# Kernel tuning notes

Measured on AMD Instinct MI355X. Metric: run time of the kernel, lower is better.

Reference implementation:

```python
import jax, jax.numpy as jnp
import numpy as np

EMBED = 2048
NH = 16          # query heads (x2 for diff pairs)
NKV = 8          # kv heads
DEPTH = 12
HD = EMBED // NH // 2   # 64
NREP = NH // NKV        # 2
SCALING = HD ** -0.5
LAMBDA_INIT = 1.0 - 0.65 * float(np.exp(-0.35 * DEPTH))
EPS = 1e-5


def setup_inputs() -> dict:
    key = jax.random.key(0)
    ks = jax.random.split(key, 12)
    T, B = 2048, 2
    x = jax.random.normal(ks[0], (T, B, EMBED), jnp.float32)
    # interleaved rotary tables over full head_dim (HD), HD/2 frequencies
    inv_freq = 1.0 / (10000.0 ** (np.arange(0, HD, 2, dtype=np.float32) / HD))
    ang = np.arange(T, dtype=np.float32)[:, None] * inv_freq[None, :]  # (T, HD/2)
    cos = jnp.asarray(np.cos(ang), jnp.float32)
    sin = jnp.asarray(np.sin(ang), jnp.float32)
    s = EMBED ** -0.5
    Wq = jax.random.normal(ks[1], (EMBED, EMBED), jnp.float32) * s
    Wk = jax.random.normal(ks[2], (EMBED, EMBED // NREP), jnp.float32) * s
    Wv = jax.random.normal(ks[3], (EMBED, EMBED // NREP), jnp.float32) * s
    Wo = jax.random.normal(ks[4], (EMBED, EMBED), jnp.float32) * s
    lq1 = jax.random.normal(ks[5], (HD,), jnp.float32) * 0.1
    lk1 = jax.random.normal(ks[6], (HD,), jnp.float32) * 0.1
    lq2 = jax.random.normal(ks[7], (HD,), jnp.float32) * 0.1
    lk2 = jax.random.normal(ks[8], (HD,), jnp.float32) * 0.1
    g = jnp.ones((2 * HD,), jnp.float32)  # RMSNorm affine weight
    return {"x": x, "cos": cos, "sin": sin, "Wq": Wq, "Wk": Wk, "Wv": Wv,
            "Wo": Wo, "lq1": lq1, "lk1": lk1, "lq2": lq2, "lk2": lk2, "g": g}


def _rope_interleaved(t, cos, sin):
    # t: (B, T, H, HD); cos/sin: (T, HD/2). Pairs are (even, odd) lanes.
    x1 = t[..., 0::2]
    x2 = t[..., 1::2]
    c = cos[None, :, None, :]
    s = sin[None, :, None, :]
    o1 = x1 * c - x2 * s
    o2 = x1 * s + x2 * c
    return jnp.stack([o1, o2], axis=-1).reshape(t.shape)


def reference(x, cos, sin, Wq, Wk, Wv, Wo, lq1, lk1, lq2, lk2, g):
    T, B, E = x.shape
    # projections (torch code reshapes (T,B,E) contiguously into (B,T,...))
    q = (x @ Wq).reshape(B, T, 2 * NH, HD)
    k = (x @ Wk).reshape(B, T, 2 * NKV, HD)
    v = (x @ Wv).reshape(B, T, NKV, 2 * HD)
    q = _rope_interleaved(q, cos, sin)
    k = _rope_interleaved(k, cos, sin)
    q = jnp.transpose(q, (0, 2, 1, 3)) * SCALING      # (B, 2NH, T, HD)
    k = jnp.repeat(jnp.transpose(k, (0, 2, 1, 3)), NREP, axis=1)  # (B, 2NH, T, HD)
    v = jnp.repeat(jnp.transpose(v, (0, 2, 1, 3)), NREP, axis=1)  # (B, NH, T, 2HD)
    aw = jnp.einsum('bhtd,bhsd->bhts', q, k)          # (B, 2NH, T, T)
    mask = jnp.triu(jnp.full((T, T), -jnp.inf, aw.dtype), 1)
    aw = jax.nn.softmax(jnp.nan_to_num(aw) + mask, axis=-1)
    lam = jnp.exp(jnp.sum(lq1 * lk1)) - jnp.exp(jnp.sum(lq2 * lk2)) + LAMBDA_INIT
    aw = aw.reshape(B, NH, 2, T, T)
    diff = aw[:, :, 0] - lam * aw[:, :, 1]            # (B, NH, T, T)
    attn = jnp.einsum('bhts,bhsd->bhtd', diff, v)     # (B, NH, T, 2HD)
    # sublayer RMSNorm over 2*HD, then scale by (1 - lambda_init)
    rms = jnp.sqrt(jnp.mean(attn * attn, axis=-1, keepdims=True) + EPS)
    attn = (attn / rms) * g * (1.0 - LAMBDA_INIT)
    attn = jnp.transpose(attn, (0, 2, 1, 3)).reshape(B, T, NH * 2 * HD)
    return attn @ Wo  # (B, T, E)
```

## Files before the change

kernel.cpp:

```cpp
#include <hip/hip_runtime.h>
#include <math.h>

typedef __attribute__((ext_vector_type(4))) float f32x4;
typedef __attribute__((ext_vector_type(8))) short short8;
typedef __attribute__((ext_vector_type(4))) short short4v;

#define LAM_INIT 0.9902528750666895f
#define ONE_M_LI 0.0097471249333105f
#define QSCALE   0.18033688011112042f

static __device__ __forceinline__ float bs2f(short s) {
  union { unsigned u; float f; } c;
  c.u = ((unsigned)(unsigned short)s) << 16;
  return c.f;
}
static __device__ __forceinline__ short f2bs(float f) {
  union { float f; unsigned u; } c; c.f = f;
  unsigned r = c.u + 0x7fffu + ((c.u >> 16) & 1u);
  return (short)(r >> 16);
}
static __device__ __forceinline__ short f2bs_fast(float f) {
  union { float f; unsigned u; } c; c.f = f;
  return (short)((c.u + 0x8000u) >> 16);
}
static __device__ __forceinline__ void gld16(const void* g, void* l) {
  __builtin_amdgcn_global_load_lds(
      (const __attribute__((address_space(1))) void*)g,
      (__attribute__((address_space(3))) void*)l, 16, 0, 0);
}
#if __has_builtin(__builtin_amdgcn_exp2f)
#define EXP2F(x) __builtin_amdgcn_exp2f(x)
#else
#define EXP2F(x) exp2f(x)
#endif

__global__ void cast_x(const float* __restrict__ x, short* __restrict__ xb, int n) {
  int i = (blockIdx.x * 256 + threadIdx.x) * 4;
  if (i < n) {
    float4 v = *(const float4*)(x + i);
    short4v o;
    o[0] = f2bs(v.x); o[1] = f2bs(v.y); o[2] = f2bs(v.z); o[3] = f2bs(v.w);
    *(short4v*)(xb + i) = o;
  }
}

__global__ void transpose_cast(const float* __restrict__ src, short* __restrict__ dst,
                               int srcCols, int dstRowOff, int dstLd) {
  __shared__ float tile[32][33];
  int c0 = blockIdx.x * 32, r0 = blockIdx.y * 32;
  int tx = threadIdx.x, ty = threadIdx.y;
#pragma unroll
  for (int i = 0; i < 32; i += 8)
    tile[ty + i][tx] = src[(long)(r0 + ty + i) * srcCols + c0 + tx];
  __syncthreads();
#pragma unroll
  for (int i = 0; i < 32; i += 8)
    dst[(long)(dstRowOff + c0 + ty + i) * dstLd + r0 + tx] = f2bs(tile[tx][ty + i]);
}

template<int BF16OUT>
__global__ __launch_bounds__(256)
void gemm_bt(const short* __restrict__ A, const short* __restrict__ Bt,
             void* __restrict__ Cp, int K, int N) {
  __shared__ __align__(16) short As[128 * 32];
  __shared__ __align__(16) short Bs[128 * 32];
  const int tid  = threadIdx.x;
  const int lane = tid & 63;
  const int wave = tid >> 6;
  const long mBase = (long)blockIdx.y * 128;
  const long nBase = (long)blockIdx.x * 128;
  const int wm = (wave >> 1) * 64;
  const int wn = (wave & 1) * 64;

  f32x4 acc[4][4];
#pragma unroll
  for (int i = 0; i < 4; i++)
#pragma unroll
    for (int j = 0; j < 4; j++)
#pragma unroll
      for (int r = 0; r < 4; r++) acc[i][j][r] = 0.f;

  const int r0  = tid >> 2;
  const int kp0 = (tid & 3) * 8;
  const short* a0 = A  + (mBase + r0) * K + kp0;
  const short* a1 = A  + (mBase + r0 + 64) * K + kp0;
  const short* b0 = Bt + (nBase + r0) * K + kp0;
  const short* b1 = Bt + (nBase + r0 + 64) * K + kp0;
  short* AsW = As + wave * 512;
  short* BsW = Bs + wave * 512;

  const int mr = wm + (lane & 15);
  const int nr = wn + (lane & 15);
  const int kr = (lane >> 4) * 8;

  for (int kt = 0; kt < K; kt += 32) {
    __syncthreads();
    gld16(a0 + kt, AsW);
    gld16(a1 + kt, AsW + 2048);
    gld16(b0 + kt, BsW);
    gld16(b1 + kt, BsW + 2048);
    __syncthreads();
    short8 af[4], bf[4];
#pragma unroll
    for (int mt = 0; mt < 4; mt++) af[mt] = *(const short8*)&As[(mr + mt * 16) * 32 + kr];
#pragma unroll
    for (int nt = 0; nt < 4; nt++) bf[nt] = *(const short8*)&Bs[(nr + nt * 16) * 32 + kr];
#pragma unroll
    for (int mt = 0; mt < 4; mt++)
#pragma unroll
      for (int nt = 0; nt < 4; nt++)
        acc[mt][nt] = __builtin_amdgcn_mfma_f32_16x16x32_bf16(af[mt], bf[nt], acc[mt][nt], 0, 0, 0);
  }

  const long col0 = nBase + wn + (lane & 15);
  const long row0 = mBase + wm + (lane >> 4) * 4;
#pragma unroll
  for (int mt = 0; mt < 4; mt++)
#pragma unroll
    for (int nt = 0; nt < 4; nt++)
#pragma unroll
      for (int rg = 0; rg < 4; rg++) {
        long idx = (row0 + mt * 16 + rg) * N + col0 + nt * 16;
        if (BF16OUT) ((short*)Cp)[idx] = f2bs(acc[mt][nt][rg]);
        else         ((float*)Cp)[idx] = acc[mt][nt][rg];
      }
}

__global__ __launch_bounds__(256) void rope_q(short* __restrict__ QKV,
    const float* __restrict__ cosp, const float* __restrict__ sinp) {
  int idx = blockIdx.x * 256 + threadIdx.x;
  int r = idx >> 8;
  int col = (idx & 255) * 8;
  short* p = QKV + (long)r * 4096 + col;
  short8 v = *(const short8*)p;
  int pos = r & 2047;
  int f0 = (col & 63) >> 1;
  float4 c = *(const float4*)(cosp + pos * 32 + f0);
  float4 s = *(const float4*)(sinp + pos * 32 + f0);
  float cc[4] = {c.x, c.y, c.z, c.w};
  float ss[4] = {s.x, s.y, s.z, s.w};
  short8 o;
#pragma unroll
  for (int j = 0; j < 4; j++) {
    float x0 = bs2f(v[2 * j]), x1 = bs2f(v[2 * j + 1]);
    o[2 * j]     = f2bs((x0 * cc[j] - x1 * ss[j]) * QSCALE);
    o[2 * j + 1] = f2bs((x0 * ss[j] + x1 * cc[j]) * QSCALE);
  }
  *(short8*)p = o;
}

__global__ __launch_bounds__(256) void repack_k(const short* __restrict__ QKV,
    const float* __restrict__ cosp, const float* __restrict__ sinp,
    short* __restrict__ Kt) {
  const int stile = blockIdx.x, h = blockIdx.y, b = blockIdx.z;
  short* dst = Kt + (long)((b * 16 + h) * 32 + stile) * 4096;
#pragma unroll
  for (int half = 0; half < 2; half++) {
    int o8 = threadIdx.x + half * 256;
    int r = o8 & 15, c = (o8 >> 4) & 3, ks = (o8 >> 6) & 1, gq = o8 >> 7;
    int t = stile * 64 + gq * 16 + r;
    const short* src = QKV + ((long)(b * 2048 + t)) * 4096 + 2048 + h * 64 + ks * 32 + c * 8;
    short8 v = *(const short8*)src;
    const float* cp = cosp + t * 32 + ks * 16 + c * 4;
    const float* sp = sinp + t * 32 + ks * 16 + c * 4;
    short8 o;
#pragma unroll
    for (int j = 0; j < 4; j++) {
      float x0 = bs2f(v[2 * j]), x1 = bs2f(v[2 * j + 1]);
      o[2 * j]     = f2bs(x0 * cp[j] - x1 * sp[j]);
      o[2 * j + 1] = f2bs(x0 * sp[j] + x1 * cp[j]);
    }
    *(short8*)(dst + o8 * 8) = o;
  }
}

__global__ __launch_bounds__(256) void repack_v(const short* __restrict__ QKV,
                                                short* __restrict__ Vt) {
  __shared__ short Ts[64][130];
  const int tid = threadIdx.x;
  const int stile = blockIdx.x, kv = blockIdx.y, b = blockIdx.z;
#pragma unroll
  for (int half = 0; half < 2; half++) {
    int trow = half * 32 + (tid >> 3);
    int hwc = (tid & 7) * 16;
    const short* src = QKV + ((long)(b * 2048 + stile * 64 + trow)) * 4096 + 3072 + kv * 128 + hwc;
    *(short8*)&Ts[trow][hwc]     = *(const short8*)src;
    *(short8*)&Ts[trow][hwc + 8] = *(const short8*)(src + 8);
  }
  __syncthreads();
  short* dst = Vt + (long)((b * 8 + kv) * 32 + stile) * 8192;
#pragma unroll
  for (int k4 = 0; k4 < 4; k4++) {
    int o8 = tid + k4 * 256;
    int r = o8 & 15, c = (o8 >> 4) & 3, ks = (o8 >> 6) & 1, gq = o8 >> 7;
    int tt = ks * 32 + c * 8;
    int dv = gq * 16 + r;
    short8 o;
#pragma unroll
    for (int j = 0; j < 8; j++) o[j] = Ts[tt + j][dv];
    *(short8*)(dst + o8 * 8) = o;
  }
}

__global__ __launch_bounds__(256, 2)
void diffattn(const short* __restrict__ QKV, const short* __restrict__ Kt,
              const short* __restrict__ Vt,
              const float* __restrict__ lq1, const float* __restrict__ lk1,
              const float* __restrict__ lq2, const float* __restrict__ lk2,
              const float* __restrict__ g, short* __restrict__ attnp) {
  __shared__ __align__(16) short Ks[2][4096];
  __shared__ __align__(16) short Vs[2][8192];
  __shared__ __align__(16) short Ps[4][2][16][72];

  const int tid  = threadIdx.x;
  const int lane = tid & 63;
  const int wave = tid >> 6;
  const int quad = lane >> 4;
  const int l15  = lane & 15;

  const int bx   = blockIdx.x;
  const int xcd  = bx & 7;
  const int slot = bx >> 3;
  const int hb   = xcd * 4 + (slot & 3);
  const int h    = hb & 15;
  const int b    = hb >> 4;
  const int qb   = 31 - (slot >> 2);
  const long rowBase = (long)b * 2048;

  float lam;
  {
    float v1 = lq1[lane] * lk1[lane];
    float v2 = lq2[lane] * lk2[lane];
#pragma unroll
    for (int m = 32; m >= 1; m >>= 1) { v1 += __shfl_xor(v1, m); v2 += __shfl_xor(v2, m); }
    lam = __expf(v1) - __expf(v2) + LAM_INIT;
  }

  const int tq = qb * 64 + wave * 16 + l15;
  short8 qf[2][2];
#pragma unroll
  for (int hd = 0; hd < 2; hd++)
#pragma unroll
    for (int ks = 0; ks < 2; ks++)
      qf[hd][ks] = *(const short8*)(QKV + (rowBase + tq) * 4096 + (2 * h + hd) * 64 + ks * 32 + quad * 8);

  const short* KtB = Kt + (long)((b * 16 + h) * 32) * 4096;
  const short* VtB = Vt + (long)((b * 8 + (h >> 1)) * 32) * 8192;
  short* KsB = &Ks[0][0];
  short* VsB = &Vs[0][0];

#define STAGE(ST, BUF) do {                                                  \
    const short* kg_ = KtB + (long)(ST) * 4096 + wave * 1024 + lane * 8;     \
    const short* vg_ = VtB + (long)(ST) * 8192 + wave * 2048 + lane * 8;     \
    short* kl_ = KsB + (BUF) * 4096 + wave * 1024;                           \
    short* vl_ = VsB + (BUF) * 8192 + wave * 2048;                           \
    gld16(kg_,        kl_);                                                  \
    gld16(kg_ + 512,  kl_ + 512);                                            \
    gld16(vg_,        vl_);                                                  \
    gld16(vg_ + 512,  vl_ + 512);                                            \
    gld16(vg_ + 1024, vl_ + 1024);                                           \
    gld16(vg_ + 1536, vl_ + 1536);                                           \
  } while (0)

  float lS[2][4];
  f32x4 oA[2][8];
#pragma unroll
  for (int hd = 0; hd < 2; hd++) {
#pragma unroll
    for (int r = 0; r < 4; r++) lS[hd][r] = 0.f;
#pragma unroll
    for (int ot = 0; ot < 8; ot++)
#pragma unroll
      for (int r = 0; r < 4; r++) oA[hd][ot][r] = 0.f;
  }

  STAGE(0, 0);

  for (int st = 0; st <= qb; st++) {
    const int buf = st & 1;
    __syncthreads();
    if (st < qb) STAGE(st + 1, buf ^ 1);

    const short* Ktile = KsB + buf * 4096;
    const short* Vtile = VsB + buf * 8192;

    f32x4 sc[2][4];
#pragma unroll
    for (int hd = 0; hd < 2; hd++)
#pragma unroll
      for (int nt = 0; nt < 4; nt++)
#pragma unroll
        for (int r = 0; r < 4; r++) sc[hd][nt][r] = 0.f;
#pragma unroll
    for (int ks = 0; ks < 2; ks++) {
      short8 kf[4];
#pragma unroll
      for (int nt = 0; nt < 4; nt++)
        kf[nt] = *(const short8*)(Ktile + (nt * 2 + ks) * 512 + lane * 8);
#pragma unroll
      for (int nt = 0; nt < 4; nt++) {
        sc[0][nt] = __builtin_amdgcn_mfma_f32_16x16x32_bf16(qf[0][ks], kf[nt], sc[0][nt], 0, 0, 0);
        sc[1][nt] = __builtin_amdgcn_mfma_f32_16x16x32_bf16(qf[1][ks], kf[nt], sc[1][nt], 0, 0, 0);
      }
    }

    const bool diag = (st == qb);
    const int tg = qb * 64 + wave * 16 + quad * 4;
#pragma unroll
    for (int hd = 0; hd < 2; hd++)
#pragma unroll
      for (int nt = 0; nt < 4; nt++) {
        const int sg = st * 64 + nt * 16 + l15;
#pragma unroll
        for (int r = 0; r < 4; r++) {
          float p = EXP2F(sc[hd][nt][r]);
          if (diag && (sg > tg + r)) p = 0.f;
          lS[hd][r] += p;
          Ps[wave][hd][quad * 4 + r][nt * 16 + l15] = f2bs_fast(p);
        }
      }

#pragma unroll
    for (int ks = 0; ks < 2; ks++) {
      short8 p0 = *(const short8*)&Ps[wave][0][l15][ks * 32 + quad * 8];
      short8 p1 = *(const short8*)&Ps[wave][1][l15][ks * 32 + quad * 8];
#pragma unroll
      for (int ot = 0; ot < 8; ot++) {
        short8 vf = *(const short8*)(Vtile + (ot * 2 + ks) * 512 + lane * 8);
        oA[0][ot] = __builtin_amdgcn_mfma_f32_16x16x32_bf16(p0, vf, oA[0][ot], 0, 0, 0);
        oA[1][ot] = __builtin_amdgcn_mfma_f32_16x16x32_bf16(p1, vf, oA[1][ot], 0, 0, 0);
      }
    }
  }
#undef STAGE

#pragma unroll
  for (int hd = 0; hd < 2; hd++)
#pragma unroll
    for (int r = 0; r < 4; r++) {
      float t = lS[hd][r];
      t += __shfl_xor(t, 1); t += __shfl_xor(t, 2);
      t += __shfl_xor(t, 4); t += __shfl_xor(t, 8);
      lS[hd][r] = t;
    }
  float i1[4], i2[4], ssq[4];
#pragma unroll
  for (int r = 0; r < 4; r++) { i1[r] = 1.f / lS[0][r]; i2[r] = lam / lS[1][r]; ssq[r] = 0.f; }
#pragma unroll
  for (int ot = 0; ot < 8; ot++)
#pragma unroll
    for (int r = 0; r < 4; r++) {
      float d = oA[0][ot][r] * i1[r] - oA[1][ot][r] * i2[r];
      oA[0][ot][r] = d;
      ssq[r] += d * d;
    }
#pragma unroll
  for (int r = 0; r < 4; r++) {
    float t = ssq[r];
    t += __shfl_xor(t, 1); t += __shfl_xor(t, 2);
    t += __shfl_xor(t, 4); t += __shfl_xor(t, 8);
    ssq[r] = ONE_M_LI / sqrtf(t * (1.f / 128.f) + 1e-5f);
  }
  const long orow = rowBase + qb * 64 + wave * 16 + quad * 4;
#pragma unroll
  for (int ot = 0; ot < 8; ot++) {
    const float gv = g[ot * 16 + l15];
#pragma unroll
    for (int r = 0; r < 4; r++)
      attnp[(orow + r) * 2048 + h * 128 + ot * 16 + l15] = f2bs(oA[0][ot][r] * ssq[r] * gv);
  }
}

extern "C" void kernel_launch(void* const* d_in, const int* in_sizes, int n_in,
                              void* d_out, int out_size, void* d_ws, size_t ws_size,
                              hipStream_t stream) {
  const float* x    = (const float*)d_in[0];
  const float* cosp = (const float*)d_in[1];
  const float* sinp = (const float*)d_in[2];
  const float* Wq   = (const float*)d_in[3];
  const float* Wk   = (const float*)d_in[4];
  const float* Wv   = (const float*)d_in[5];
  const float* Wo   = (const float*)d_in[6];
  const float* lq1  = (const float*)d_in[7];
  const float* lk1  = (const float*)d_in[8];
  const float* lq2  = (const float*)d_in[9];
  const float* lk2  = (const float*)d_in[10];
  const float* g    = (const float*)d_in[11];
  float* out = (float*)d_out;

  const size_t MB = 1u << 20;
  char* ws = (char*)d_ws;
  short* xb    = (short*)(ws);
  short* Kt    = (short*)(ws);
  short* Vt    = (short*)(ws + 8 * MB);
  short* Wqkvt = (short*)(ws + 16 * MB);
  short* Wot   = (short*)(ws + 32 * MB);
  short* QKVb  = (short*)(ws + 40 * MB);
  short* attnp = (short*)(ws + 72 * MB);

  cast_x<<<8192, 256, 0, stream>>>(x, xb, 8388608);
  dim3 tb(32, 8);
  transpose_cast<<<dim3(64, 64), tb, 0, stream>>>(Wq, Wqkvt, 2048, 0, 2048);
  transpose_cast<<<dim3(32, 64), tb, 0, stream>>>(Wk, Wqkvt, 1024, 2048, 2048);
  transpose_cast<<<dim3(32, 64), tb, 0, stream>>>(Wv, Wqkvt, 1024, 3072, 2048);
  transpose_cast<<<dim3(64, 64), tb, 0, stream>>>(Wo, Wot, 2048, 0, 2048);

  gemm_bt<1><<<dim3(32, 32), 256, 0, stream>>>(xb, Wqkvt, QKVb, 2048, 4096);
  rope_q<<<4096, 256, 0, stream>>>(QKVb, cosp, sinp);
  repack_k<<<dim3(32, 16, 2), 256, 0, stream>>>(QKVb, cosp, sinp, Kt);
  repack_v<<<dim3(32, 8, 2), 256, 0, stream>>>(QKVb, Vt);
  diffattn<<<1024, 256, 0, stream>>>(QKVb, Kt, Vt, lq1, lk1, lq2, lk2, g, attnp);
  gemm_bt<0><<<dim3(16, 32), 256, 0, stream>>>(attnp, Wot, out, 2048, 2048);
}
```

Before: 382.3 us.

## Merge weight transposes and K/V repacks, add XCD-aware GEMM tile mapping

```diff
diff --git a/kernel.cpp b/kernel.cpp
--- a/kernel.cpp
+++ b/kernel.cpp
@@ -44,9 +44,16 @@
   }
 }
 
-__global__ void transpose_cast(const float* __restrict__ src, short* __restrict__ dst,
-                               int srcCols, int dstRowOff, int dstLd) {
+__global__ void transpose_all(const float* __restrict__ Wq, const float* __restrict__ Wk,
+                              const float* __restrict__ Wv, const float* __restrict__ Wo,
+                              short* __restrict__ Wqkvt, short* __restrict__ Wot) {
   __shared__ float tile[32][33];
+  const int z = blockIdx.z;
+  const int srcCols = (z == 1 || z == 2) ? 1024 : 2048;
+  if (blockIdx.x * 32 >= srcCols) return;
+  const float* src = (z == 0) ? Wq : (z == 1) ? Wk : (z == 2) ? Wv : Wo;
+  short* dst = (z == 3) ? Wot : Wqkvt;
+  const int dstRowOff = (z == 1) ? 2048 : (z == 2) ? 3072 : 0;
   int c0 = blockIdx.x * 32, r0 = blockIdx.y * 32;
   int tx = threadIdx.x, ty = threadIdx.y;
 #pragma unroll
@@ -55,20 +62,24 @@
   __syncthreads();
 #pragma unroll
   for (int i = 0; i < 32; i += 8)
-    dst[(long)(dstRowOff + c0 + ty + i) * dstLd + r0 + tx] = f2bs(tile[tx][ty + i]);
+    dst[(long)(dstRowOff + c0 + ty + i) * 2048 + r0 + tx] = f2bs(tile[tx][ty + i]);
 }
 
 template<int BF16OUT>
 __global__ __launch_bounds__(256)
 void gemm_bt(const short* __restrict__ A, const short* __restrict__ Bt,
-             void* __restrict__ Cp, int K, int N) {
+             void* __restrict__ Cp, int K, int N,
+             int bxMask, int bxShift, int bandH) {
   __shared__ __align__(16) short As[128 * 32];
   __shared__ __align__(16) short Bs[128 * 32];
   const int tid  = threadIdx.x;
   const int lane = tid & 63;
   const int wave = tid >> 6;
-  const long mBase = (long)blockIdx.y * 128;
-  const long nBase = (long)blockIdx.x * 128;
+  const int bid  = blockIdx.x;
+  const int xcd  = bid & 7;
+  const int s    = bid >> 3;
+  const long mBase = (long)(xcd * bandH + (s >> bxShift)) * 128;
+  const long nBase = (long)(s & bxMask) * 128;
   const int wm = (wave >> 1) * 64;
   const int wn = (wave & 1) * 64;
 
@@ -149,56 +160,56 @@
   *(short8*)p = o;
 }
 
-__global__ __launch_bounds__(256) void repack_k(const short* __restrict__ QKV,
+__global__ __launch_bounds__(256) void repack_kv(const short* __restrict__ QKV,
     const float* __restrict__ cosp, const float* __restrict__ sinp,
-    short* __restrict__ Kt) {
-  const int stile = blockIdx.x, h = blockIdx.y, b = blockIdx.z;
-  short* dst = Kt + (long)((b * 16 + h) * 32 + stile) * 4096;
-#pragma unroll
-  for (int half = 0; half < 2; half++) {
-    int o8 = threadIdx.x + half * 256;
-    int r = o8 & 15, c = (o8 >> 4) & 3, ks = (o8 >> 6) & 1, gq = o8 >> 7;
-    int t = stile * 64 + gq * 16 + r;
-    const short* src = QKV + ((long)(b * 2048 + t)) * 4096 + 2048 + h * 64 + ks * 32 + c * 8;
-    short8 v = *(const short8*)src;
-    const float* cp = cosp + t * 32 + ks * 16 + c * 4;
-    const float* sp = sinp + t * 32 + ks * 16 + c * 4;
-    short8 o;
-#pragma unroll
-    for (int j = 0; j < 4; j++) {
-      float x0 = bs2f(v[2 * j]), x1 = bs2f(v[2 * j + 1]);
-      o[2 * j]     = f2bs(x0 * cp[j] - x1 * sp[j]);
-      o[2 * j + 1] = f2bs(x0 * sp[j] + x1 * cp[j]);
-    }
-    *(short8*)(dst + o8 * 8) = o;
-  }
-}
-
-__global__ __launch_bounds__(256) void repack_v(const short* __restrict__ QKV,
-                                                short* __restrict__ Vt) {
-  __shared__ short Ts[64][130];
-  const int tid = threadIdx.x;
-  const int stile = blockIdx.x, kv = blockIdx.y, b = blockIdx.z;
-#pragma unroll
-  for (int half = 0; half < 2; half++) {
-    int trow = half * 32 + (tid >> 3);
-    int hwc = (tid & 7) * 16;
-    const short* src = QKV + ((long)(b * 2048 + stile * 64 + trow)) * 4096 + 3072 + kv * 128 + hwc;
-    *(short8*)&Ts[trow][hwc]     = *(const short8*)src;
-    *(short8*)&Ts[trow][hwc + 8] = *(const short8*)(src + 8);
-  }
-  __syncthreads();
-  short* dst = Vt + (long)((b * 8 + kv) * 32 + stile) * 8192;
-#pragma unroll
-  for (int k4 = 0; k4 < 4; k4++) {
-    int o8 = tid + k4 * 256;
-    int r = o8 & 15, c = (o8 >> 4) & 3, ks = (o8 >> 6) & 1, gq = o8 >> 7;
-    int tt = ks * 32 + c * 8;
-    int dv = gq * 16 + r;
-    short8 o;
-#pragma unroll
-    for (int j = 0; j < 8; j++) o[j] = Ts[tt + j][dv];
-    *(short8*)(dst + o8 * 8) = o;
+    short* __restrict__ Kt, short* __restrict__ Vt) {
+  const int stile = blockIdx.x, b = blockIdx.z;
+  if (blockIdx.y < 16) {
+    const int h = blockIdx.y;
+    short* dst = Kt + (long)((b * 16 + h) * 32 + stile) * 4096;
+#pragma unroll
+    for (int half = 0; half < 2; half++) {
+      int o8 = threadIdx.x + half * 256;
+      int r = o8 & 15, c = (o8 >> 4) & 3, ks = (o8 >> 6) & 1, gq = o8 >> 7;
+      int t = stile * 64 + gq * 16 + r;
+      const short* src = QKV + ((long)(b * 2048 + t)) * 4096 + 2048 + h * 64 + ks * 32 + c * 8;
+      short8 v = *(const short8*)src;
+      const float* cp = cosp + t * 32 + ks * 16 + c * 4;
+      const float* sp = sinp + t * 32 + ks * 16 + c * 4;
+      short8 o;
+#pragma unroll
+      for (int j = 0; j < 4; j++) {
+        float x0 = bs2f(v[2 * j]), x1 = bs2f(v[2 * j + 1]);
+        o[2 * j]     = f2bs(x0 * cp[j] - x1 * sp[j]);
+        o[2 * j + 1] = f2bs(x0 * sp[j] + x1 * cp[j]);
+      }
+      *(short8*)(dst + o8 * 8) = o;
+    }
+  } else {
+    __shared__ short Ts[64][130];
+    const int tid = threadIdx.x;
+    const int kv = blockIdx.y - 16;
+#pragma unroll
+    for (int half = 0; half < 2; half++) {
+      int trow = half * 32 + (tid >> 3);
+      int hwc = (tid & 7) * 16;
+      const short* src = QKV + ((long)(b * 2048 + stile * 64 + trow)) * 4096 + 3072 + kv * 128 + hwc;
+      *(short8*)&Ts[trow][hwc]     = *(const short8*)src;
+      *(short8*)&Ts[trow][hwc + 8] = *(const short8*)(src + 8);
+    }
+    __syncthreads();
+    short* dst = Vt + (long)((b * 8 + kv) * 32 + stile) * 8192;
+#pragma unroll
+    for (int k4 = 0; k4 < 4; k4++) {
+      int o8 = tid + k4 * 256;
+      int r = o8 & 15, c = (o8 >> 4) & 3, ks = (o8 >> 6) & 1, gq = o8 >> 7;
+      int tt = ks * 32 + c * 8;
+      int dv = gq * 16 + r;
+      short8 o;
+#pragma unroll
+      for (int j = 0; j < 8; j++) o[j] = Ts[tt + j][dv];
+      *(short8*)(dst + o8 * 8) = o;
+    }
   }
 }
 
@@ -399,16 +410,11 @@
   short* attnp = (short*)(ws + 72 * MB);
 
   cast_x<<<8192, 256, 0, stream>>>(x, xb, 8388608);
-  dim3 tb(32, 8);
-  transpose_cast<<<dim3(64, 64), tb, 0, stream>>>(Wq, Wqkvt, 2048, 0, 2048);
-  transpose_cast<<<dim3(32, 64), tb, 0, stream>>>(Wk, Wqkvt, 1024, 2048, 2048);
-  transpose_cast<<<dim3(32, 64), tb, 0, stream>>>(Wv, Wqkvt, 1024, 3072, 2048);
-  transpose_cast<<<dim3(64, 64), tb, 0, stream>>>(Wo, Wot, 2048, 0, 2048);
-
-  gemm_bt<1><<<dim3(32, 32), 256, 0, stream>>>(xb, Wqkvt, QKVb, 2048, 4096);
+  transpose_all<<<dim3(64, 64, 4), dim3(32, 8), 0, stream>>>(Wq, Wk, Wv, Wo, Wqkvt, Wot);
+
+  gemm_bt<1><<<1024, 256, 0, stream>>>(xb, Wqkvt, QKVb, 2048, 4096, 31, 5, 4);
   rope_q<<<4096, 256, 0, stream>>>(QKVb, cosp, sinp);
-  repack_k<<<dim3(32, 16, 2), 256, 0, stream>>>(QKVb, cosp, sinp, Kt);
-  repack_v<<<dim3(32, 8, 2), 256, 0, stream>>>(QKVb, Vt);
+  repack_kv<<<dim3(32, 24, 2), 256, 0, stream>>>(QKVb, cosp, sinp, Kt, Vt);
   diffattn<<<1024, 256, 0, stream>>>(QKVb, Kt, Vt, lq1, lk1, lq2, lk2, g, attnp);
-  gemm_bt<0><<<dim3(16, 32), 256, 0, stream>>>(attnp, Wot, out, 2048, 2048);
-}
+  gemm_bt<0><<<512, 256, 0, stream>>>(attnp, Wot, out, 2048, 2048, 15, 4, 4);
+}
```

Result: no change. 376.7 us (-1.5%).
